# Kernel optimization log

Measured on AMD Instinct MI355X. Metric: run time of the kernel, lower is better.

## Reference

```python
import jax, jax.numpy as jnp
import numpy as np

H, C, G = 4, 32, 64          # heads, per-head channels, num graphs
D_IN, HID = 128, 128          # input feature dim, dueling MLP hidden
NEG_SLOPE = 0.2               # GATv2Conv default negative_slope


def setup_inputs() -> dict:
    key = jax.random.key(0)
    ks = jax.random.split(key, 16)
    N, E = 50000, 800000
    x = jax.random.normal(ks[0], (N, D_IN), jnp.float32)
    edge_index = jax.random.randint(ks[1], (2, E), 0, N, dtype=jnp.int64)
    batch = jnp.sort(jax.random.randint(ks[2], (N,), 0, G, dtype=jnp.int64))
    s_in = 1.0 / np.sqrt(D_IN)
    s_g = 1.0 / np.sqrt(H * C)
    s_h = 1.0 / np.sqrt(HID)
    return {
        "x": x,
        "W_l": jax.random.normal(ks[3], (D_IN, H * C), jnp.float32) * s_in,
        "b_l": jnp.zeros((H * C,), jnp.float32),
        "W_r": jax.random.normal(ks[4], (D_IN, H * C), jnp.float32) * s_in,
        "b_r": jnp.zeros((H * C,), jnp.float32),
        "att": jax.random.normal(ks[5], (H, C), jnp.float32) * (1.0 / np.sqrt(C)),
        "bias": jnp.zeros((H * C,), jnp.float32),
        "Wq1": jax.random.normal(ks[6], (H * C, HID), jnp.float32) * s_g,
        "bq1": jnp.zeros((HID,), jnp.float32),
        "Wq2": jax.random.normal(ks[7], (HID, 2), jnp.float32) * s_h,
        "bq2": jnp.zeros((2,), jnp.float32),
        "Wv1": jax.random.normal(ks[8], (H * C, HID), jnp.float32) * s_g,
        "bv1": jnp.zeros((HID,), jnp.float32),
        "Wv2": jax.random.normal(ks[9], (HID, 1), jnp.float32) * s_h,
        "bv2": jnp.zeros((1,), jnp.float32),
        "edge_index": edge_index,
        "batch": batch,
    }


def reference(x, W_l, b_l, W_r, b_r, att, bias,
              Wq1, bq1, Wq2, bq2, Wv1, bv1, Wv2, bv2,
              edge_index, batch):
    N = x.shape[0]
    # add self loops (PyG GATv2Conv default)
    loop = jnp.arange(N, dtype=edge_index.dtype)
    src = jnp.concatenate([edge_index[0], loop])  # message source j
    dst = jnp.concatenate([edge_index[1], loop])  # aggregation target i

    xl = (x @ W_l + b_l).reshape(N, H, C)  # source transform
    xr = (x @ W_r + b_r).reshape(N, H, C)  # target transform

    # per-edge GATv2 score: a^T LeakyReLU(xl_j + xr_i), shape [Et, H]
    m = jax.nn.leaky_relu(xl[src] + xr[dst], NEG_SLOPE)
    e = jnp.einsum('ehc,hc->eh', m, att)

    # segment softmax over incoming edges of each target node
    emax = jax.ops.segment_max(e, dst, num_segments=N)
    ee = jnp.exp(e - emax[dst])
    denom = jax.ops.segment_sum(ee, dst, num_segments=N)
    alpha = ee / (denom[dst] + 1e-16)  # [Et, H]

    # scatter-add weighted source features, concat heads
    out = jax.ops.segment_sum(alpha[:, :, None] * xl[src], dst, num_segments=N)
    h = jax.nn.relu(out.reshape(N, H * C) + bias)

    # global max pool per graph
    g = jax.ops.segment_max(h, batch, num_segments=G)  # [G, H*C]

    # dueling heads
    q = jax.nn.relu(g @ Wq1 + bq1) @ Wq2 + bq2  # [G, 2]
    v = jax.nn.relu(g @ Wv1 + bv1) @ Wv2 + bv2  # [G, 1]
    return q - q.mean(axis=1, keepdims=True) + v
```

## Files before the change

### kernel.cpp

```cpp
#include <hip/hip_runtime.h>
#include <hip/hip_fp16.h>

#define F   128
#define DIN 128
#define HID 128
#define NEG 0.2f
#define L2E 1.4426950408889634f
#define KNODE 8
#define CAP  64
#define CSTR 16

typedef _Float16 hvec2 __attribute__((ext_vector_type(2)));
typedef _Float16 half8 __attribute__((ext_vector_type(8)));
typedef float f32x4 __attribute__((ext_vector_type(4)));
union U2 { unsigned u; hvec2 v; };
union UH { _Float16 f; unsigned short u; };

template<int CTRL>
__device__ __forceinline__ float dpp_addf(float x){
    int t = __builtin_amdgcn_update_dpp(0, __float_as_int(x), CTRL, 0xF, 0xF, true);
    return x + __int_as_float(t);
}

__global__ void k_prep(const float* __restrict__ Wl, const float* __restrict__ Wr,
                       const float* __restrict__ att,
                       const float* __restrict__ bl, const float* __restrict__ br,
                       unsigned short* __restrict__ WT, unsigned* __restrict__ att_h,
                       float* __restrict__ bcat){
    const int e = blockIdx.x * 256 + threadIdx.x;
    if (e < 32768){
        const int k = e >> 8, col = e & 255;
        const float w = (col < 128) ? Wl[k * 128 + col] : Wr[k * 128 + (col - 128)];
        UH u; u.f = (_Float16)w;
        WT[col * 128 + k] = u.u;
    }
    if (e < 64){
        float2 a2 = ((const float2*)att)[e];
        U2 r; r.v = hvec2{(_Float16)(a2.x * L2E), (_Float16)(a2.y * L2E)};
        att_h[e] = r.u;
    }
    if (e < 256) bcat[e] = (e < 128) ? bl[e] : br[e - 128];
}

__global__ void k_scatter(const int* __restrict__ ei, unsigned* __restrict__ cnt,
                          int* __restrict__ slots, int E){
    int t = blockIdx.x * blockDim.x + threadIdx.x;
    if (t >= E) return;
    const int dst = ei[E + t];
    const unsigned pos = atomicAdd(&cnt[(size_t)dst * CSTR], 1u);
    if (pos < CAP - 1) slots[((size_t)dst << 6) + 1 + pos] = ei[t];
}

__global__ __launch_bounds__(256) void k_mm(const float* __restrict__ x,
                      const unsigned short* __restrict__ WT, const float* __restrict__ bcat,
                      unsigned short* __restrict__ xl_s, unsigned short* __restrict__ xr_s,
                      int N){
    const int t = threadIdx.x;
    const int w = t >> 6, lane = t & 63;
    const int li = lane & 15, hi = lane >> 4;
    const int rowA = blockIdx.x * 64 + w * 16 + li;
    const int rA = (rowA < N) ? rowA : N - 1;
    f32x4 acc[16];
    #pragma unroll
    for (int c = 0; c < 16; ++c) acc[c] = f32x4{0.f, 0.f, 0.f, 0.f};
    #pragma unroll
    for (int kt = 0; kt < 4; ++kt){
        const int k0 = kt * 32 + hi * 8;
        const float4 f0 = *(const float4*)(x + (size_t)rA * DIN + k0);
        const float4 f1 = *(const float4*)(x + (size_t)rA * DIN + k0 + 4);
        half8 b;
        b[0] = (_Float16)f0.x; b[1] = (_Float16)f0.y; b[2] = (_Float16)f0.z; b[3] = (_Float16)f0.w;
        b[4] = (_Float16)f1.x; b[5] = (_Float16)f1.y; b[6] = (_Float16)f1.z; b[7] = (_Float16)f1.w;
        #pragma unroll
        for (int c = 0; c < 16; ++c){
            const half8 a = *(const half8*)(WT + (size_t)(c * 16 + li) * 128 + k0);
            acc[c] = __builtin_amdgcn_mfma_f32_16x16x32_f16(a, b, acc[c], 0, 0, 0);
        }
    }
    if (rowA < N){
        #pragma unroll
        for (int c = 0; c < 16; ++c){
            const int col0 = c * 16 + hi * 4;
            const float4 bv = *(const float4*)(bcat + col0);
            UH p0, p1, p2, p3;
            p0.f = (_Float16)(acc[c][0] + bv.x);
            p1.f = (_Float16)(acc[c][1] + bv.y);
            p2.f = (_Float16)(acc[c][2] + bv.z);
            p3.f = (_Float16)(acc[c][3] + bv.w);
            uint2 val;
            val.x = (unsigned)p0.u | ((unsigned)p1.u << 16);
            val.y = (unsigned)p2.u | ((unsigned)p3.u << 16);
            if (col0 < 128) *(uint2*)(xl_s + (size_t)rowA * F + col0)         = val;
            else            *(uint2*)(xr_s + (size_t)rowA * F + (col0 - 128)) = val;
        }
    }
}

__global__ void k_node(const unsigned* __restrict__ xl_h, const unsigned* __restrict__ xr_h,
                       const int* __restrict__ slots, const unsigned* __restrict__ cnt,
                       const unsigned* __restrict__ att_h, const float* __restrict__ bias,
                       const int* __restrict__ batch, unsigned* __restrict__ g_bits, int N){
    const int wid  = (int)(((long long)blockIdx.x * blockDim.x + threadIdx.x) >> 6);
    const int lane = threadIdx.x & 63;
    const int i0 = wid * KNODE;
    if (i0 >= N) return;
    U2 atv; atv.u = att_h[lane];
    const float2 bz = ((const float2*)bias)[lane];
    const hvec2 neg2 = {(_Float16)NEG, (_Float16)NEG};
    float pool0 = 0.f, pool1 = 0.f;
    int curg = __builtin_amdgcn_readfirstlane(batch[i0]);
    const int iend = (i0 + KNODE < N) ? i0 + KNODE : N;

    for (int i = i0; i < iend; ++i){
        const int g = __builtin_amdgcn_readfirstlane(batch[i]);
        if (g != curg){
            atomicMax(&g_bits[curg * F + 2 * lane],     __float_as_uint(pool0));
            atomicMax(&g_bits[curg * F + 2 * lane + 1], __float_as_uint(pool1));
            pool0 = 0.f; pool1 = 0.f; curg = g;
        }
        const int rs = i << 6;
        int dt = (int)cnt[(size_t)i * CSTR] + 1;
        if (dt > CAP) dt = CAP;
        U2 xrv; xrv.u = xr_h[(size_t)i * 64 + lane];

        float d0=0.f,d1=0.f,d2=0.f,d3=0.f,d4=0.f,d5=0.f,d6=0.f,d7=0.f;
        float ax0=0.f,ax1=0.f,ax2=0.f,ax3=0.f,ax4=0.f,ax5=0.f,ax6=0.f,ax7=0.f;
        float ay0=0.f,ay1=0.f,ay2=0.f,ay3=0.f,ay4=0.f,ay5=0.f,ay6=0.f,ay7=0.f;

        auto proc = [&](unsigned hv, float& d_, float& ax_, float& ay_){
            U2 xlv; xlv.u = hv;
            hvec2 z = xlv.v + xrv.v;
            hvec2 r = __builtin_elementwise_max(z, z * neg2);
#if __has_builtin(__builtin_amdgcn_fdot2)
            float s = __builtin_amdgcn_fdot2(r, atv.v, 0.f, false);
#else
            float s = fmaf((float)r.x, (float)atv.v.x, (float)r.y * (float)atv.v.y);
#endif
            s = dpp_addf<0xB1>(s);
            s = dpp_addf<0x4E>(s);
            s = dpp_addf<0x124>(s);
            s = dpp_addf<0x128>(s);
            const float p = exp2f(s);
            d_ += p;
            ax_ = fmaf(p, (float)xlv.v.x, ax_);
            ay_ = fmaf(p, (float)xlv.v.y, ay_);
        };

        const int my_src = (lane > 0 && lane < dt) ? slots[rs + lane] : i;
        int e = 0;
        for (; e + 7 < dt; e += 8){
            const int s0 = __builtin_amdgcn_readlane(my_src, e);
            const int s1 = __builtin_amdgcn_readlane(my_src, e + 1);
            const int s2 = __builtin_amdgcn_readlane(my_src, e + 2);
            const int s3 = __builtin_amdgcn_readlane(my_src, e + 3);
            const int s4 = __builtin_amdgcn_readlane(my_src, e + 4);
            const int s5 = __builtin_amdgcn_readlane(my_src, e + 5);
            const int s6 = __builtin_amdgcn_readlane(my_src, e + 6);
            const int s7 = __builtin_amdgcn_readlane(my_src, e + 7);
            const unsigned h0 = xl_h[(size_t)s0 * 64 + lane];
            const unsigned h1 = xl_h[(size_t)s1 * 64 + lane];
            const unsigned h2 = xl_h[(size_t)s2 * 64 + lane];
            const unsigned h3 = xl_h[(size_t)s3 * 64 + lane];
            const unsigned h4 = xl_h[(size_t)s4 * 64 + lane];
            const unsigned h5 = xl_h[(size_t)s5 * 64 + lane];
            const unsigned h6 = xl_h[(size_t)s6 * 64 + lane];
            const unsigned h7 = xl_h[(size_t)s7 * 64 + lane];
            proc(h0, d0, ax0, ay0); proc(h1, d1, ax1, ay1);
            proc(h2, d2, ax2, ay2); proc(h3, d3, ax3, ay3);
            proc(h4, d4, ax4, ay4); proc(h5, d5, ax5, ay5);
            proc(h6, d6, ax6, ay6); proc(h7, d7, ax7, ay7);
        }
        for (; e + 3 < dt; e += 4){
            const int s0 = __builtin_amdgcn_readlane(my_src, e);
            const int s1 = __builtin_amdgcn_readlane(my_src, e + 1);
            const int s2 = __builtin_amdgcn_readlane(my_src, e + 2);
            const int s3 = __builtin_amdgcn_readlane(my_src, e + 3);
            const unsigned h0 = xl_h[(size_t)s0 * 64 + lane];
            const unsigned h1 = xl_h[(size_t)s1 * 64 + lane];
            const unsigned h2 = xl_h[(size_t)s2 * 64 + lane];
            const unsigned h3 = xl_h[(size_t)s3 * 64 + lane];
            proc(h0, d0, ax0, ay0); proc(h1, d1, ax1, ay1);
            proc(h2, d2, ax2, ay2); proc(h3, d3, ax3, ay3);
        }
        for (; e < dt; ++e){
            const int s0 = __builtin_amdgcn_readlane(my_src, e);
            proc(xl_h[(size_t)s0 * 64 + lane], d0, ax0, ay0);
        }

        const float dsum = ((d0 + d1) + (d2 + d3)) + ((d4 + d5) + (d6 + d7));
        const float ax = ((ax0 + ax1) + (ax2 + ax3)) + ((ax4 + ax5) + (ax6 + ax7));
        const float ay = ((ay0 + ay1) + (ay2 + ay3)) + ((ay4 + ay5) + (ay6 + ay7));
        const float inv = 1.f / (dsum + 1e-16f);
        pool0 = fmaxf(pool0, fmaxf(fmaf(ax, inv, bz.x), 0.f));
        pool1 = fmaxf(pool1, fmaxf(fmaf(ay, inv, bz.y), 0.f));
    }
    atomicMax(&g_bits[curg * F + 2 * lane],     __float_as_uint(pool0));
    atomicMax(&g_bits[curg * F + 2 * lane + 1], __float_as_uint(pool1));
}

__global__ void k_dueling(const float* __restrict__ g,
                          const float* __restrict__ Wq1, const float* __restrict__ bq1,
                          const float* __restrict__ Wq2, const float* __restrict__ bq2,
                          const float* __restrict__ Wv1, const float* __restrict__ bv1,
                          const float* __restrict__ Wv2, const float* __restrict__ bv2,
                          float* __restrict__ out){
    __shared__ float gs[F], red0[128], red1[128], red2[128];
    const int t = threadIdx.x, gi = blockIdx.x;
    gs[t] = g[gi * F + t];
    __syncthreads();
    float aq = bq1[t], av = bv1[t];
    for (int k = 0; k < F; ++k){
        aq = fmaf(gs[k], Wq1[k * HID + t], aq);
        av = fmaf(gs[k], Wv1[k * HID + t], av);
    }
    aq = aq > 0.f ? aq : 0.f;
    av = av > 0.f ? av : 0.f;
    red0[t] = aq * Wq2[t * 2 + 0];
    red1[t] = aq * Wq2[t * 2 + 1];
    red2[t] = av * Wv2[t];
    __syncthreads();
    for (int off = 64; off > 0; off >>= 1){
        if (t < off){ red0[t] += red0[t + off]; red1[t] += red1[t + off]; red2[t] += red2[t + off]; }
        __syncthreads();
    }
    if (t == 0){
        const float q0 = red0[0] + bq2[0];
        const float q1 = red1[0] + bq2[1];
        const float v  = red2[0] + bv2[0];
        out[gi * 2 + 0] = 0.5f * (q0 - q1) + v;
        out[gi * 2 + 1] = 0.5f * (q1 - q0) + v;
    }
}

extern "C" void kernel_launch(void* const* d_in, const int* in_sizes, int n_in,
                              void* d_out, int out_size, void* d_ws, size_t ws_size,
                              hipStream_t stream) {
    const float* x    = (const float*)d_in[0];
    const float* Wl   = (const float*)d_in[1];
    const float* bl   = (const float*)d_in[2];
    const float* Wr   = (const float*)d_in[3];
    const float* br   = (const float*)d_in[4];
    const float* att  = (const float*)d_in[5];
    const float* bias = (const float*)d_in[6];
    const float* Wq1  = (const float*)d_in[7];
    const float* bq1  = (const float*)d_in[8];
    const float* Wq2  = (const float*)d_in[9];
    const float* bq2  = (const float*)d_in[10];
    const float* Wv1  = (const float*)d_in[11];
    const float* bv1  = (const float*)d_in[12];
    const float* Wv2  = (const float*)d_in[13];
    const float* bv2  = (const float*)d_in[14];
    const int*   ei   = (const int*)d_in[15];
    const int*   batch= (const int*)d_in[16];
    float* out = (float*)d_out;

    const int N  = in_sizes[0] / DIN;
    const int E  = in_sizes[15] / 2;
    const int Gg = out_size / 2;
    const int GF = Gg * F;

    unsigned* xl_h   = (unsigned*)d_ws;
    unsigned* xr_h   = xl_h + (size_t)N * 64;
    unsigned* att_h  = xr_h + (size_t)N * 64;
    unsigned* WT     = att_h + 64;
    float*    bcat   = (float*)(WT + 16384);
    unsigned* cnt    = (unsigned*)(bcat + 256);
    unsigned* g_bits = cnt + (size_t)N * CSTR;
    int*      slots  = (int*)(g_bits + GF);

    (void)hipMemsetAsync(cnt, 0, ((size_t)N * CSTR + GF) * sizeof(unsigned), stream);
    k_prep<<<128, 256, 0, stream>>>(Wl, Wr, att, bl, br, (unsigned short*)WT, att_h, bcat);
    k_scatter<<<(E + 255) / 256, 256, 0, stream>>>(ei, cnt, slots, E);
    k_mm<<<(N + 63) / 64, 256, 0, stream>>>(x, (const unsigned short*)WT, bcat,
                                            (unsigned short*)xl_h, (unsigned short*)xr_h, N);
    {
        const long long waves = (N + KNODE - 1) / KNODE;
        const long long thr = waves * 64;
        k_node<<<(unsigned)((thr + 255) / 256), 256, 0, stream>>>(
            xl_h, xr_h, slots, cnt, att_h, bias, batch, g_bits, N);
    }
    k_dueling<<<Gg, 128, 0, stream>>>((const float*)g_bits, Wq1, bq1, Wq2, bq2,
                                      Wv1, bv1, Wv2, bv2, out);
}
```

Measured before the change: 171.3 us.

## Replace per-node atomic scatter with two-pass bucketed binning into node slots

Edges are first binned into buckets of 64 destination nodes with one global atomic counter per bucket, packing src and the low dst bits into one word. A second kernel per bucket then counts and places edges into per-node slots using shared-memory atomics. This replaces scattered global atomics on padded per-node counters, which caused contention and poor locality, with a compact count array. The cost is an extra kernel launch and an extra pass over a bucket buffer. The packing assumes src fits in 26 bits, and each bucket holds at most CAPB edges.

```diff
diff --git a/kernel.cpp b/kernel.cpp
--- a/kernel.cpp
+++ b/kernel.cpp
@@ -8,7 +8,8 @@
 #define L2E 1.4426950408889634f
 #define KNODE 8
 #define CAP  64
-#define CSTR 16
+#define BW   64
+#define CAPB 1536
 
 typedef _Float16 hvec2 __attribute__((ext_vector_type(2)));
 typedef _Float16 half8 __attribute__((ext_vector_type(8)));
@@ -42,13 +43,35 @@
     if (e < 256) bcat[e] = (e < 128) ? bl[e] : br[e - 128];
 }
 
-__global__ void k_scatter(const int* __restrict__ ei, unsigned* __restrict__ cnt,
-                          int* __restrict__ slots, int E){
+__global__ void k_bin(const int* __restrict__ ei, unsigned* __restrict__ bcnt,
+                      unsigned* __restrict__ bucket, int E){
     int t = blockIdx.x * blockDim.x + threadIdx.x;
     if (t >= E) return;
+    const int src = ei[t];
     const int dst = ei[E + t];
-    const unsigned pos = atomicAdd(&cnt[(size_t)dst * CSTR], 1u);
-    if (pos < CAP - 1) slots[((size_t)dst << 6) + 1 + pos] = ei[t];
+    const int b = dst >> 6;
+    const unsigned pos = atomicAdd(&bcnt[b], 1u);
+    if (pos < CAPB) bucket[(size_t)b * CAPB + pos] = ((unsigned)src << 6) | (unsigned)(dst & 63);
+}
+
+__global__ __launch_bounds__(256) void k_bsc(const unsigned* __restrict__ bcnt,
+                     const unsigned* __restrict__ bucket, unsigned* __restrict__ cnt,
+                     int* __restrict__ slots, int N){
+    __shared__ unsigned lc[BW];
+    const int b = blockIdx.x;
+    const int t = threadIdx.x;
+    if (t < BW) lc[t] = 0u;
+    __syncthreads();
+    const int base = b << 6;
+    int n = (int)bcnt[b]; if (n > CAPB) n = CAPB;
+    for (int e = t; e < n; e += 256){
+        const unsigned w = bucket[(size_t)b * CAPB + e];
+        const int d = (int)(w & 63u);
+        const unsigned pos = atomicAdd(&lc[d], 1u);
+        if (pos < CAP - 1) slots[((size_t)(base + d) << 6) + 1 + pos] = (int)(w >> 6);
+    }
+    __syncthreads();
+    if (t < BW && base + t < N) cnt[base + t] = lc[t];
 }
 
 __global__ __launch_bounds__(256) void k_mm(const float* __restrict__ x,
@@ -119,7 +142,7 @@
             pool0 = 0.f; pool1 = 0.f; curg = g;
         }
         const int rs = i << 6;
-        int dt = (int)cnt[(size_t)i * CSTR] + 1;
+        int dt = (int)cnt[i] + 1;
         if (dt > CAP) dt = CAP;
         U2 xrv; xrv.u = xr_h[(size_t)i * 64 + lane];
 
@@ -258,19 +281,23 @@
     const int E  = in_sizes[15] / 2;
     const int Gg = out_size / 2;
     const int GF = Gg * F;
+    const int NBK = (N + BW - 1) / BW;
 
     unsigned* xl_h   = (unsigned*)d_ws;
     unsigned* xr_h   = xl_h + (size_t)N * 64;
     unsigned* att_h  = xr_h + (size_t)N * 64;
     unsigned* WT     = att_h + 64;
     float*    bcat   = (float*)(WT + 16384);
-    unsigned* cnt    = (unsigned*)(bcat + 256);
-    unsigned* g_bits = cnt + (size_t)N * CSTR;
+    unsigned* bcnt   = (unsigned*)(bcat + 256);
+    unsigned* cnt    = bcnt + NBK;
+    unsigned* g_bits = cnt + N;
     int*      slots  = (int*)(g_bits + GF);
-
-    (void)hipMemsetAsync(cnt, 0, ((size_t)N * CSTR + GF) * sizeof(unsigned), stream);
+    unsigned* bucket = (unsigned*)(slots + (size_t)N * 64);
+
+    (void)hipMemsetAsync(bcnt, 0, (size_t)(NBK + N + GF) * sizeof(unsigned), stream);
     k_prep<<<128, 256, 0, stream>>>(Wl, Wr, att, bl, br, (unsigned short*)WT, att_h, bcat);
-    k_scatter<<<(E + 255) / 256, 256, 0, stream>>>(ei, cnt, slots, E);
+    k_bin<<<(E + 255) / 256, 256, 0, stream>>>(ei, bcnt, bucket, E);
+    k_bsc<<<NBK, 256, 0, stream>>>(bcnt, bucket, cnt, slots, N);
     k_mm<<<(N + 63) / 64, 256, 0, stream>>>(x, (const unsigned short*)WT, bcat,
                                             (unsigned short*)xl_h, (unsigned short*)xr_h, N);
     {
```

Measured after the change: 326.1 us. 1.9x slower.
